# Performance work log

Hardware: AMD Instinct MI355X
Metric: run time of the kernel (lower is better)

The kernel has to match this reference:

```python
import jax, jax.numpy as jnp
import numpy as np

TAU = 10.0
EPS = 1e-6
TOP_K = 8


def setup_inputs() -> dict:
    key = jax.random.key(0)
    ks = jax.random.split(key, 5)
    D, NB, H = 1024, 512, 4096
    B, S = 4, 2048
    x = jax.random.normal(ks[0], (B, S, D), dtype=jnp.float32)
    W1 = jax.random.normal(ks[1], (H, D), dtype=jnp.float32) * (1.0 / np.sqrt(D))
    W2 = jax.random.normal(ks[2], (D, H), dtype=jnp.float32) * (1.0 / np.sqrt(H))
    ln_g = jnp.ones((D,), jnp.float32)
    ln_b = jnp.zeros((D,), jnp.float32)
    router_W = jax.random.normal(ks[3], (NB, D), dtype=jnp.float32) * 0.01
    router_b = jnp.zeros((NB,), jnp.float32)
    raw_U = jax.random.normal(ks[4], (NB, D), dtype=jnp.float32) * 0.02
    raw_V = jax.random.normal(jax.random.fold_in(key, 7), (NB, D), dtype=jnp.float32) * 0.02
    gamma = jnp.ones((1, 1, D), jnp.float32) * 0.1
    return {"x": x, "W1": W1, "W2": W2, "ln_g": ln_g, "ln_b": ln_b,
            "router_W": router_W, "router_b": router_b,
            "raw_U": raw_U, "raw_V": raw_V, "gamma": gamma}


def _layernorm(x, g, b):
    mu = jnp.mean(x, axis=-1, keepdims=True)
    var = jnp.var(x, axis=-1, keepdims=True)
    return (x - mu) * jax.lax.rsqrt(var + 1e-5) * g + b


def _unit_rows(W):
    n = jnp.linalg.norm(W, axis=1, keepdims=True)
    return W / jnp.maximum(n, EPS)


def reference(x, W1, W2, ln_g, ln_b, router_W, router_b, raw_U, raw_V, gamma):
    B, S, D = x.shape
    x_flat = x.reshape(-1, D)                      # [N, D]
    r_raw = _layernorm(x_flat, ln_g, ln_b) @ router_W.T + router_b  # [N, NB]
    r = jnp.clip(r_raw, -TAU, TAU)
    alpha = jax.nn.softplus(r)
    phi, idx = jax.lax.top_k(alpha, TOP_K)         # [N, K]
    S_sum = jnp.sum(phi, axis=-1, keepdims=True)
    Z = (phi / (S_sum + EPS)) * jnp.tanh(S_sum)    # [N, K]
    U_sel = _unit_rows(raw_U)[idx]                 # [N, K, D]
    V_sel = _unit_rows(raw_V)[idx]                 # [N, K, D]
    h_lat = jnp.einsum('nd,nkd->nk', x_flat, U_sel)
    dyn = jnp.einsum('nk,nkd->nd', h_lat * Z, V_sel).reshape(B, S, D) * gamma
    static = (jax.nn.gelu(x_flat @ W1.T, approximate=False) @ W2.T).reshape(B, S, D)
    return static + dyn
```

## Files before the change

### kernel.cpp

```cpp
#include <hip/hip_runtime.h>
#include <hip/hip_bf16.h>
#include <math.h>

#define N_TOK 8192
#define DDIM  1024
#define HDIM  4096
#define NBLK  512

typedef __bf16 bf16x8 __attribute__((ext_vector_type(8)));
typedef __bf16 bf16x4 __attribute__((ext_vector_type(4)));
typedef float  floatx4 __attribute__((ext_vector_type(4)));

__device__ __forceinline__ float wave_reduce_sum(float v) {
#pragma unroll
    for (int off = 32; off > 0; off >>= 1) v += __shfl_down(v, off, 64);
    return v;
}

__device__ __forceinline__ void gload_lds16(const void* g, void* l) {
    __builtin_amdgcn_global_load_lds((const __attribute__((address_space(1))) void*)g,
                                     (__attribute__((address_space(3))) void*)l,
                                     16, 0, 0);
}

__device__ __forceinline__ float fast_gelu(float x) {
    float ax = fabsf(x);
    float z  = ax * 0.70710678118654752f;
    float t  = __builtin_amdgcn_rcpf(fmaf(0.3275911f, z, 1.0f));
    float p  = fmaf(fmaf(fmaf(fmaf(1.061405429f, t, -1.453152027f),
                              t, 1.421413741f),
                         t, -0.284496736f),
                    t, 0.254829592f);
    p *= t;
    float e = __expf(-z * z);
    float E = fmaf(-p, e, 1.0f);
    return 0.5f * fmaf(ax, E, x);
}

__device__ __forceinline__ float fast_softplus(float r) {
    return __logf(fmaf(1.0f, __expf(r), 1.0f));
}

__device__ __forceinline__ void cast1024(const float* __restrict__ s,
                                         __bf16* __restrict__ d,
                                         size_t off, int t) {
    float4 v = ((const float4*)(s + off))[t];
    bf16x4 o;
    o.x = (__bf16)v.x; o.y = (__bf16)v.y;
    o.z = (__bf16)v.z; o.w = (__bf16)v.w;
    ((bf16x4*)(d + off))[t] = o;
}

__global__ __launch_bounds__(256) void prep_kernel(
        const float* __restrict__ x,
        const float* __restrict__ ln_g, const float* __restrict__ ln_b,
        const float* __restrict__ W1,   const float* __restrict__ W2,
        const float* __restrict__ router_W,
        const float* __restrict__ rawU, const float* __restrict__ rawV,
        __bf16* __restrict__ xb,  __bf16* __restrict__ lnb,
        __bf16* __restrict__ w1b, __bf16* __restrict__ w2b,
        __bf16* __restrict__ rwb,
        float* __restrict__ unitU, float* __restrict__ unitV) {
    int b = blockIdx.x;
    int t = threadIdx.x;

    if (b < 1024) {
        const float* src = (b < NBLK) ? rawU + (size_t)b * DDIM
                                      : rawV + (size_t)(b - NBLK) * DDIM;
        float* dst = (b < NBLK) ? unitU + (size_t)b * DDIM
                                : unitV + (size_t)(b - NBLK) * DDIM;
        float vals[4];
        float ss = 0.f;
#pragma unroll
        for (int i = 0; i < 4; i++) { vals[i] = src[t + i * 256]; ss += vals[i] * vals[i]; }
        __shared__ float red[4];
        ss = wave_reduce_sum(ss);
        if ((t & 63) == 0) red[t >> 6] = ss;
        __syncthreads();
        float tot = red[0] + red[1] + red[2] + red[3];
        float inv = 1.f / fmaxf(sqrtf(tot), 1e-6f);
#pragma unroll
        for (int i = 0; i < 4; i++) dst[t + i * 256] = vals[i] * inv;
    } else if (b < 9216) {
        int n = b - 1024;
        const float* row = x + (size_t)n * DDIM;
        float v[4];
        float s1 = 0.f, s2 = 0.f;
#pragma unroll
        for (int i = 0; i < 4; i++) {
            v[i] = row[t + i * 256];
            s1 += v[i];
            s2 += v[i] * v[i];
        }
        __shared__ float r1[4], r2[4];
        s1 = wave_reduce_sum(s1);
        s2 = wave_reduce_sum(s2);
        if ((t & 63) == 0) { r1[t >> 6] = s1; r2[t >> 6] = s2; }
        __syncthreads();
        float mu  = (r1[0] + r1[1] + r1[2] + r1[3]) * (1.f / DDIM);
        float var = (r2[0] + r2[1] + r2[2] + r2[3]) * (1.f / DDIM) - mu * mu;
        float rstd = rsqrtf(var + 1e-5f);
        __bf16* orow = lnb + (size_t)n * DDIM;
        __bf16* xrow = xb  + (size_t)n * DDIM;
#pragma unroll
        for (int i = 0; i < 4; i++) {
            int d = t + i * 256;
            orow[d] = (__bf16)((v[i] - mu) * rstd * ln_g[d] + ln_b[d]);
            xrow[d] = (__bf16)v[i];
        }
    } else if (b < 13312) {
        cast1024(W1, w1b, (size_t)(b - 9216) * 1024, t);
    } else if (b < 17408) {
        cast1024(W2, w2b, (size_t)(b - 13312) * 1024, t);
    } else {
        cast1024(router_W, rwb, (size_t)(b - 17408) * 1024, t);
    }
}

template <int MODE, int BN>
__global__ __launch_bounds__(256) void mfma_gemm(const __bf16* __restrict__ A,
                                                 const __bf16* __restrict__ B,
                                                 const float* __restrict__ bias,
                                                 void* __restrict__ Cv,
                                                 int M, int Nn, int Kk) {
    constexpr int NJ  = BN / 32;
    constexpr int NQB = BN / 64;
    __shared__ __align__(16) __bf16 As[2][128 * 32];
    __shared__ __align__(16) __bf16 Bs[2][BN * 32];

    const int t    = threadIdx.x;
    const int lane = t & 63;
    const int wave = t >> 6;
    const int wm   = wave >> 1, wn = wave & 1;
    const int lr   = lane & 15, quad = lane >> 4;
    const int m0   = blockIdx.x * 128;
    const int n0   = blockIdx.y * BN;

    const int ca0 = t & 3;
    const __bf16* Ag[2];
    const __bf16* Bg[NQB];
    int ldsOffA[2], ldsOffB[NQB];
#pragma unroll
    for (int q = 0; q < 2; q++) {
        int idx = q * 256 + t;
        Ag[q]      = A + (size_t)(m0 + (idx >> 2)) * Kk + ca0 * 8;
        ldsOffA[q] = idx * 8;
    }
#pragma unroll
    for (int q = 0; q < NQB; q++) {
        int idx = q * 256 + t;
        Bg[q]      = B + (size_t)(n0 + (idx >> 2)) * Kk + ca0 * 8;
        ldsOffB[q] = idx * 8;
    }

    int raOff[4], rbOff[NJ];
#pragma unroll
    for (int i = 0; i < 4; i++)
        raOff[i] = (wm * 64 + i * 16 + lr) * 32 + quad * 8;
#pragma unroll
    for (int j = 0; j < NJ; j++)
        rbOff[j] = (wn * (BN / 2) + j * 16 + lr) * 32 + quad * 8;

    floatx4 acc[4][NJ];
#pragma unroll
    for (int i = 0; i < 4; i++)
#pragma unroll
        for (int j = 0; j < NJ; j++) acc[i][j] = (floatx4)0.f;

#pragma unroll
    for (int q = 0; q < 2; q++)   gload_lds16(Ag[q], &As[0][ldsOffA[q]]);
#pragma unroll
    for (int q = 0; q < NQB; q++) gload_lds16(Bg[q], &Bs[0][ldsOffB[q]]);

    const int niter = Kk >> 5;
    for (int it = 0; it < niter; ++it) {
        const int cur = it & 1;
        __syncthreads();
        if (it + 1 < niter) {
            const int nk = (it + 1) << 5;
            const int nb = cur ^ 1;
#pragma unroll
            for (int q = 0; q < 2; q++)   gload_lds16(Ag[q] + nk, &As[nb][ldsOffA[q]]);
#pragma unroll
            for (int q = 0; q < NQB; q++) gload_lds16(Bg[q] + nk, &Bs[nb][ldsOffB[q]]);
        }
        bf16x8 af[4], bfr[NJ];
#pragma unroll
        for (int i = 0; i < 4; i++)  af[i]  = *(const bf16x8*)&As[cur][raOff[i]];
#pragma unroll
        for (int j = 0; j < NJ; j++) bfr[j] = *(const bf16x8*)&Bs[cur][rbOff[j]];
#pragma unroll
        for (int i = 0; i < 4; i++)
#pragma unroll
            for (int j = 0; j < NJ; j++)
                acc[i][j] = __builtin_amdgcn_mfma_f32_16x16x32_bf16(af[i], bfr[j],
                                                                    acc[i][j], 0, 0, 0);
    }

    const int mBase = m0 + wm * 64 + quad * 4;
    const int nBase = n0 + wn * (BN / 2) + lr;
#pragma unroll
    for (int i = 0; i < 4; i++) {
#pragma unroll
        for (int j = 0; j < NJ; j++) {
            int n = nBase + j * 16;
#pragma unroll
            for (int r = 0; r < 4; r++) {
                int m = mBase + i * 16 + r;
                float v = acc[i][j][r];
                if (MODE == 0) {
                    float rr = v + bias[n];
                    rr = fminf(fmaxf(rr, -10.f), 10.f);
                    ((float*)Cv)[(size_t)m * Nn + n] = fast_softplus(rr);
                } else if (MODE == 1) {
                    ((__bf16*)Cv)[(size_t)m * Nn + n] = (__bf16)fast_gelu(v);
                } else {
                    ((float*)Cv)[(size_t)m * Nn + n] += v;
                }
            }
        }
    }
}

__global__ __launch_bounds__(256) void topk_dyn_kernel(
        const float* __restrict__ alpha,
        const float* __restrict__ x,
        const float* __restrict__ unitU,
        const float* __restrict__ unitV,
        const float* __restrict__ gamma,
        float* __restrict__ out) {
    int n = blockIdx.x;
    int t = threadIdx.x;
    int lane = t & 63, wid = t >> 6;

    __shared__ int   sidx[8];
    __shared__ float shz[8];
    __shared__ float red[8][4];
    __shared__ float hz[8];

    if (wid == 0) {
        const float* row = alpha + (size_t)n * NBLK;
        float v[8];
#pragma unroll
        for (int i = 0; i < 8; i++) v[i] = row[lane + i * 64];
        float topv[8];
        int   topi[8];
        for (int s = 0; s < 8; s++) {
            float bv = v[0]; int bi = 0;
#pragma unroll
            for (int i = 1; i < 8; i++)
                if (v[i] > bv) { bv = v[i]; bi = i; }
            int gidx = lane + bi * 64;
#pragma unroll
            for (int off = 1; off < 64; off <<= 1) {
                float ov = __shfl_xor(bv, off, 64);
                int   oi = __shfl_xor(gidx, off, 64);
                if (ov > bv || (ov == bv && oi < gidx)) { bv = ov; gidx = oi; }
            }
            topv[s] = bv; topi[s] = gidx;
            if ((gidx & 63) == lane) v[gidx >> 6] = -1e30f;
        }
        float S = 0.f;
#pragma unroll
        for (int s = 0; s < 8; s++) S += topv[s];
        float zscale = tanhf(S) / (S + 1e-6f);
        if (lane < 8) {
            sidx[lane] = topi[lane];
            shz[lane]  = topv[lane] * zscale;
        }
    }
    __syncthreads();

    const float* xr = x + (size_t)n * DDIM;
    float xv[4];
#pragma unroll
    for (int i = 0; i < 4; i++) xv[i] = xr[t + i * 256];

    float acc[8];
#pragma unroll
    for (int k = 0; k < 8; k++) {
        const float* ur = unitU + (size_t)sidx[k] * DDIM;
        float a = 0.f;
#pragma unroll
        for (int i = 0; i < 4; i++) a = fmaf(xv[i], ur[t + i * 256], a);
        acc[k] = a;
    }
#pragma unroll
    for (int k = 0; k < 8; k++) {
        float a = wave_reduce_sum(acc[k]);
        if (lane == 0) red[k][wid] = a;
    }
    __syncthreads();
    if (t < 8) {
        float h = red[t][0] + red[t][1] + red[t][2] + red[t][3];
        hz[t] = h * shz[t];
    }
    __syncthreads();

    float* orow = out + (size_t)n * DDIM;
#pragma unroll
    for (int i = 0; i < 4; i++) {
        int d = t + i * 256;
        float s = 0.f;
#pragma unroll
        for (int k = 0; k < 8; k++)
            s = fmaf(hz[k], unitV[(size_t)sidx[k] * DDIM + d], s);
        orow[d] = s * gamma[d];
    }
}

extern "C" void kernel_launch(void* const* d_in, const int* in_sizes, int n_in,
                              void* d_out, int out_size, void* d_ws, size_t ws_size,
                              hipStream_t stream) {
    const float* x        = (const float*)d_in[0];
    const float* W1       = (const float*)d_in[1];
    const float* W2       = (const float*)d_in[2];
    const float* ln_g     = (const float*)d_in[3];
    const float* ln_b     = (const float*)d_in[4];
    const float* router_W = (const float*)d_in[5];
    const float* router_b = (const float*)d_in[6];
    const float* raw_U    = (const float*)d_in[7];
    const float* raw_V    = (const float*)d_in[8];
    const float* gamma    = (const float*)d_in[9];
    float* out = (float*)d_out;

    char* ws = (char*)d_ws;
    __bf16* lnb   = (__bf16*)(ws);
    float*  alpha = (float*)(ws + 16777216u);
    __bf16* g1    = (__bf16*)(ws);
    __bf16* xb    = (__bf16*)(ws + 67108864u);
    __bf16* w1b   = (__bf16*)(ws + 83886080u);
    __bf16* w2b   = (__bf16*)(ws + 92274688u);
    __bf16* rwb   = (__bf16*)(ws + 100663296u);
    float*  unitU = (float*)(ws + 101711872u);
    float*  unitV = (float*)(ws + 103809024u);

    prep_kernel<<<17920, 256, 0, stream>>>(x, ln_g, ln_b, W1, W2, router_W,
                                           raw_U, raw_V, xb, lnb, w1b, w2b, rwb,
                                           unitU, unitV);

    dim3 gR(N_TOK / 128, NBLK / 64);
    mfma_gemm<0, 64><<<gR, 256, 0, stream>>>(lnb, rwb, router_b, (void*)alpha,
                                             N_TOK, NBLK, DDIM);

    topk_dyn_kernel<<<N_TOK, 256, 0, stream>>>(alpha, x, unitU, unitV, gamma, out);

    dim3 g1d(N_TOK / 128, HDIM / 128);
    mfma_gemm<1, 128><<<g1d, 256, 0, stream>>>(xb, w1b, nullptr, (void*)g1,
                                               N_TOK, HDIM, DDIM);

    dim3 g2d(N_TOK / 128, DDIM / 64);
    mfma_gemm<2, 64><<<g2d, 256, 0, stream>>>(g1, w2b, nullptr, (void*)out,
                                              N_TOK, DDIM, HDIM);
}
```

Measured before the change: 378.2 us.

## Add 8-wave 256-row MFMA GEMM with quadrant pipelining for FFN matmuls

Adds a new 512-thread GEMM kernel that computes 256xBN output tiles, stages A and B halves into double-buffered LDS in four sub-steps interleaved with MFMA quadrants, and raises wave priority around the compute. It also remaps block IDs across 8 XCD chunks to improve L2 locality. Both FFN matmuls (W1 with GELU, W2 accumulate) switch to it, aiming for more reuse per loaded tile and overlap of global loads with compute. The larger tiles raise register and LDS pressure (up to 128 KB of LDS per block) and leave fewer blocks in the grid.

```diff
diff --git a/kernel.cpp b/kernel.cpp
--- a/kernel.cpp
+++ b/kernel.cpp
@@ -213,6 +213,171 @@
                     rr = fminf(fmaxf(rr, -10.f), 10.f);
                     ((float*)Cv)[(size_t)m * Nn + n] = fast_softplus(rr);
                 } else if (MODE == 1) {
+                    ((__bf16*)Cv)[(size_t)m * Nn + n] = (__bf16)fast_gelu(v);
+                } else {
+                    ((float*)Cv)[(size_t)m * Nn + n] += v;
+                }
+            }
+        }
+    }
+}
+
+template <int MODE, int BN>
+__global__ __launch_bounds__(512, 2) void mfma_gemm8(const __bf16* __restrict__ A,
+                                                     const __bf16* __restrict__ B,
+                                                     void* __restrict__ Cv,
+                                                     int M, int Nn, int Kk) {
+    constexpr int NJH    = BN / 128;
+    constexpr int NJ     = 2 * NJH;
+    constexpr int BCALLS = BN / 128;
+
+    __shared__ __align__(16) __bf16 As[2][256 * 64];
+    __shared__ __align__(16) __bf16 Bs[2][BN * 64];
+
+    const int t    = threadIdx.x;
+    const int lane = t & 63;
+    const int wave = t >> 6;
+    const int wm   = wave >> 2;
+    const int wn   = wave & 3;
+    const int lr   = lane & 15, quad = lane >> 4;
+
+    const int nbn   = Nn / BN;
+    const int chunk = gridDim.x >> 3;
+    const int bid   = blockIdx.x;
+    const int wg    = (bid & 7) * chunk + (bid >> 3);
+    const int m0    = (wg / nbn) * 256;
+    const int n0    = (wg % nbn) * BN;
+
+    const __bf16* aSrc[2][2]; int aDst[2][2];
+#pragma unroll
+    for (int q = 0; q < 2; q++) {
+        int idx = q * 512 + t;
+        int row = idx >> 3;
+        int cb  = ((idx & 7) << 4) ^ ((row & 7) << 4);
+#pragma unroll
+        for (int mh = 0; mh < 2; mh++) {
+            aSrc[q][mh] = A + (size_t)(m0 + mh * 128 + row) * Kk + (cb >> 1);
+            aDst[q][mh] = (mh * 128 + row) * 64 + (idx & 7) * 8;
+        }
+    }
+    const __bf16* bSrc[BCALLS][2]; int bDst[BCALLS][2];
+#pragma unroll
+    for (int q = 0; q < BCALLS; q++) {
+        int idx = q * 512 + t;
+        int row = idx >> 3;
+        int cb  = ((idx & 7) << 4) ^ ((row & 7) << 4);
+#pragma unroll
+        for (int nh = 0; nh < 2; nh++) {
+            bSrc[q][nh] = B + (size_t)(n0 + nh * (BN / 2) + row) * Kk + (cb >> 1);
+            bDst[q][nh] = (nh * (BN / 2) + row) * 64 + (idx & 7) * 8;
+        }
+    }
+
+    int aRd[2], bRd[2];
+#pragma unroll
+    for (int ks = 0; ks < 2; ks++) {
+        int sw = ((ks * 64 + quad * 16) ^ ((lr & 7) << 4)) >> 1;
+        aRd[ks] = (wm * 64 + lr) * 64 + sw;
+        bRd[ks] = (wn * (BN / 8) + lr) * 64 + sw;
+    }
+
+    floatx4 acc[8][NJ];
+#pragma unroll
+    for (int i = 0; i < 8; i++)
+#pragma unroll
+        for (int j = 0; j < NJ; j++) acc[i][j] = (floatx4)0.f;
+
+    bf16x8 af[4][2];
+    bf16x8 bfr[NJH][2];
+
+#define STAGE_A(KT, MH, BUF)                                                     \
+    _Pragma("unroll") for (int q = 0; q < 2; q++)                                \
+        gload_lds16(aSrc[q][MH] + (size_t)(KT) * 64, &As[BUF][aDst[q][MH]])
+#define STAGE_B(KT, NH, BUF)                                                     \
+    _Pragma("unroll") for (int q = 0; q < BCALLS; q++)                           \
+        gload_lds16(bSrc[q][NH] + (size_t)(KT) * 64, &Bs[BUF][bDst[q][NH]])
+#define LDA(MH)                                                                  \
+    _Pragma("unroll") for (int ii = 0; ii < 4; ii++)                             \
+    _Pragma("unroll") for (int ks = 0; ks < 2; ks++)                             \
+        af[ii][ks] = *(const bf16x8*)&As[cur][aRd[ks] + (MH) * 8192 + ii * 1024]
+#define LDB(NH)                                                                  \
+    _Pragma("unroll") for (int jj = 0; jj < NJH; jj++)                           \
+    _Pragma("unroll") for (int ks = 0; ks < 2; ks++)                             \
+        bfr[jj][ks] = *(const bf16x8*)&Bs[cur][bRd[ks] + ((NH) * (BN / 2) + jj * 16) * 64]
+#define MM(MH, NH)                                                               \
+    _Pragma("unroll") for (int ii = 0; ii < 4; ii++)                             \
+    _Pragma("unroll") for (int jj = 0; jj < NJH; jj++)                           \
+    _Pragma("unroll") for (int ks = 0; ks < 2; ks++)                             \
+        acc[(MH) * 4 + ii][(NH) * NJH + jj] =                                    \
+            __builtin_amdgcn_mfma_f32_16x16x32_bf16(                             \
+                af[ii][ks], bfr[jj][ks], acc[(MH) * 4 + ii][(NH) * NJH + jj],    \
+                0, 0, 0)
+#define WAITV()                                                                  \
+    do { if constexpr (BCALLS == 2) asm volatile("s_waitcnt vmcnt(4)" ::: "memory"); \
+         else                       asm volatile("s_waitcnt vmcnt(3)" ::: "memory"); } while (0)
+#define WAITL() asm volatile("s_waitcnt lgkmcnt(0)" ::: "memory")
+#define BARR()  __builtin_amdgcn_s_barrier()
+#define PRIO1() __builtin_amdgcn_s_setprio(1)
+#define PRIO0() __builtin_amdgcn_s_setprio(0)
+
+    const int NT = Kk >> 6;
+
+    STAGE_A(0, 0, 0);
+    STAGE_B(0, 0, 0);
+    STAGE_A(0, 1, 0);
+    STAGE_B(0, 1, 0);
+    WAITV();
+    BARR();
+
+    for (int kt = 0; kt < NT; ++kt) {
+        const int cur = kt & 1;
+        const int nxt = cur ^ 1;
+        const bool st = (kt + 1 < NT);
+        LDA(0); LDB(0);
+        if (st) STAGE_A(kt + 1, 0, nxt);
+        WAITV(); BARR(); WAITL();
+        PRIO1(); MM(0, 0); PRIO0();
+        BARR();
+        LDA(1);
+        if (st) STAGE_B(kt + 1, 0, nxt);
+        WAITV(); BARR(); WAITL();
+        PRIO1(); MM(1, 0); PRIO0();
+        BARR();
+        LDB(1);
+        if (st) STAGE_A(kt + 1, 1, nxt);
+        WAITV(); BARR(); WAITL();
+        PRIO1(); MM(1, 1); PRIO0();
+        BARR();
+        LDA(0);
+        if (st) STAGE_B(kt + 1, 1, nxt);
+        WAITV(); BARR(); WAITL();
+        PRIO1(); MM(0, 1); PRIO0();
+        BARR();
+    }
+
+#undef STAGE_A
+#undef STAGE_B
+#undef LDA
+#undef LDB
+#undef MM
+#undef WAITV
+#undef WAITL
+#undef BARR
+#undef PRIO1
+#undef PRIO0
+
+#pragma unroll
+    for (int i = 0; i < 8; i++) {
+        const int mh = i >> 2, ii = i & 3;
+#pragma unroll
+        for (int j = 0; j < NJ; j++) {
+            const int nh = j / NJH, jj = j % NJH;
+            const int n = n0 + nh * (BN / 2) + wn * (BN / 8) + jj * 16 + lr;
+#pragma unroll
+            for (int r = 0; r < 4; r++) {
+                const int m = m0 + mh * 128 + wm * 64 + ii * 16 + quad * 4 + r;
+                const float v = acc[i][j][r];
+                if (MODE == 1) {
                     ((__bf16*)Cv)[(size_t)m * Nn + n] = (__bf16)fast_gelu(v);
                 } else {
                     ((float*)Cv)[(size_t)m * Nn + n] += v;
@@ -345,11 +510,9 @@
 
     topk_dyn_kernel<<<N_TOK, 256, 0, stream>>>(alpha, x, unitU, unitV, gamma, out);
 
-    dim3 g1d(N_TOK / 128, HDIM / 128);
-    mfma_gemm<1, 128><<<g1d, 256, 0, stream>>>(xb, w1b, nullptr, (void*)g1,
-                                               N_TOK, HDIM, DDIM);
-
-    dim3 g2d(N_TOK / 128, DDIM / 64);
-    mfma_gemm<2, 64><<<g2d, 256, 0, stream>>>(g1, w2b, nullptr, (void*)out,
-                                              N_TOK, DDIM, HDIM);
-}
+    mfma_gemm8<1, 256><<<dim3(512), dim3(512), 0, stream>>>(xb, w1b, (void*)g1,
+                                                            N_TOK, HDIM, DDIM);
+
+    mfma_gemm8<2, 128><<<dim3(256), dim3(512), 0, stream>>>(g1, w2b, (void*)out,
+                                                            N_TOK, DDIM, HDIM);
+}
```

New measurement: 376.3 us. About the same (-0.5%).

## Replace FFN GEMMs with 256x256 8-wave pipelined MFMA kernel and split-K

Applied to the files above, without the earlier changes.

Adds a new 512-thread GEMM kernel with 256x256 tiles, double-buffered LDS via direct global-to-LDS loads, interleaved quarter-tile MFMA phases with wave priority hints, and XCD-aware block remapping. The W1 GEMM uses it directly with GELU, and the W2 GEMM uses split-K=2 with atomic adds into the output. The aim is more data reuse per tile and better overlap of loads with MFMA, which should raise matrix-core utilisation for the two big FFN GEMMs. The cost is large register and LDS use per block, and fp32 atomics that make the summation order nondeterministic.

```diff
diff --git a/kernel.cpp b/kernel.cpp
--- a/kernel.cpp
+++ b/kernel.cpp
@@ -216,6 +216,148 @@
                     ((__bf16*)Cv)[(size_t)m * Nn + n] = (__bf16)fast_gelu(v);
                 } else {
                     ((float*)Cv)[(size_t)m * Nn + n] += v;
+                }
+            }
+        }
+    }
+}
+
+template <int MODE, int SPLITK>
+__global__ __launch_bounds__(512, 2) void mfma_gemm8v2(const __bf16* __restrict__ A,
+                                                       const __bf16* __restrict__ B,
+                                                       void* __restrict__ Cv,
+                                                       int M, int Nn, int Kk) {
+    __shared__ __align__(16) __bf16 As[2][256 * 64];
+    __shared__ __align__(16) __bf16 Bs[2][256 * 64];
+
+    const int t    = threadIdx.x;
+    const int lane = t & 63;
+    const int wave = t >> 6;
+    const int wm   = wave >> 2;
+    const int wn   = wave & 3;
+    const int lr   = lane & 15, quad = lane >> 4;
+
+    const int nbn   = Nn >> 8;
+    const int nmb   = M >> 8;
+    const int chunk = gridDim.x >> 3;
+    const int bid   = blockIdx.x;
+    const int wg    = (bid & 7) * chunk + (bid >> 3);
+    const int kslc  = wg / (nmb * nbn);
+    const int rem   = wg % (nmb * nbn);
+    const int m0    = (rem / nbn) * 256;
+    const int n0    = (rem % nbn) * 256;
+    const int kseg  = Kk / SPLITK;
+    const int NT    = kseg >> 6;
+
+    const int srow = t >> 3;
+    const int scb  = ((t & 7) << 4) ^ ((srow & 7) << 4);
+    const __bf16* aP = A + (size_t)(m0 + srow) * Kk + (size_t)kslc * kseg + (scb >> 1);
+    const __bf16* bP = B + (size_t)(n0 + srow) * Kk + (size_t)kslc * kseg + (scb >> 1);
+    const int dP = srow * 64 + (t & 7) * 8;
+
+    int aRd[2], bRd[2];
+#pragma unroll
+    for (int ks = 0; ks < 2; ks++) {
+        int sw = ((ks * 64 + quad * 16) ^ ((lr & 7) << 4)) >> 1;
+        aRd[ks] = (wm * 64 + lr) * 64 + sw;
+        bRd[ks] = (wn * 32 + lr) * 64 + sw;
+    }
+
+    floatx4 acc[8][4];
+#pragma unroll
+    for (int i = 0; i < 8; i++)
+#pragma unroll
+        for (int j = 0; j < 4; j++) acc[i][j] = (floatx4)0.f;
+
+    bf16x8 af[4][2];
+    bf16x8 bfr0[2][2];
+    bf16x8 bfr1[2][2];
+
+#define STAGE_A(KT, MH, BUF)                                                        \
+    _Pragma("unroll") for (int q = 0; q < 2; q++)                                   \
+        gload_lds16(aP + (size_t)(KT) * 64 + (size_t)(q * 64 + (MH) * 128) * Kk,    \
+                    &As[BUF][dP + (q * 64 + (MH) * 128) * 64])
+#define STAGE_B(KT, NH, BUF)                                                        \
+    _Pragma("unroll") for (int q = 0; q < 2; q++)                                   \
+        gload_lds16(bP + (size_t)(KT) * 64 + (size_t)(q * 64 + (NH) * 128) * Kk,    \
+                    &Bs[BUF][dP + (q * 64 + (NH) * 128) * 64])
+#define LDA(CUR, MH)                                                                \
+    _Pragma("unroll") for (int ii = 0; ii < 4; ii++)                                \
+    _Pragma("unroll") for (int ks = 0; ks < 2; ks++)                                \
+        af[ii][ks] = *(const bf16x8*)&As[CUR][aRd[ks] + (MH) * 8192 + ii * 1024]
+#define LDB(CUR, NH, DST)                                                           \
+    _Pragma("unroll") for (int jj = 0; jj < 2; jj++)                                \
+    _Pragma("unroll") for (int ks = 0; ks < 2; ks++)                                \
+        DST[jj][ks] = *(const bf16x8*)&Bs[CUR][bRd[ks] + ((NH) * 128 + jj * 16) * 64]
+#define MM(MH, NH, BFR)                                                             \
+    _Pragma("unroll") for (int ii = 0; ii < 4; ii++)                                \
+    _Pragma("unroll") for (int jj = 0; jj < 2; jj++)                                \
+    _Pragma("unroll") for (int ks = 0; ks < 2; ks++)                                \
+        acc[(MH) * 4 + ii][(NH) * 2 + jj] =                                         \
+            __builtin_amdgcn_mfma_f32_16x16x32_bf16(                                \
+                af[ii][ks], BFR[jj][ks], acc[(MH) * 4 + ii][(NH) * 2 + jj], 0, 0, 0)
+#define VWAIT(NSTR) asm volatile("s_waitcnt vmcnt(" NSTR ")" ::: "memory")
+#define WAITL()     asm volatile("s_waitcnt lgkmcnt(0)" ::: "memory")
+#define BARR()      __builtin_amdgcn_s_barrier()
+#define PRIO1()     __builtin_amdgcn_s_setprio(1)
+#define PRIO0()     __builtin_amdgcn_s_setprio(0)
+
+#define TILE(KT, CUR, ST1, ST2, VM0, VM1, VM3)                                      \
+    do {                                                                            \
+        LDA(CUR, 0); LDB(CUR, 0, bfr0);                                             \
+        if (ST1) { STAGE_A((KT) + 1, 1, ((KT) + 1) & 1); }                          \
+        VWAIT(VM0); BARR(); WAITL();                                                \
+        PRIO1(); MM(0, 0, bfr0); PRIO0(); BARR();                                   \
+        LDB(CUR, 1, bfr1);                                                          \
+        if (ST2) { STAGE_A((KT) + 2, 0, (KT) & 1); }                                \
+        VWAIT(VM1); BARR(); WAITL();                                                \
+        PRIO1(); MM(0, 1, bfr1); PRIO0(); BARR();                                   \
+        LDA(CUR, 1);                                                                \
+        if (ST2) { STAGE_B((KT) + 2, 0, (KT) & 1); }                                \
+        BARR(); WAITL();                                                            \
+        PRIO1(); MM(1, 1, bfr1); PRIO0(); BARR();                                   \
+        if (ST2) { STAGE_B((KT) + 2, 1, (KT) & 1); }                                \
+        VWAIT(VM3); BARR();                                                         \
+        PRIO1(); MM(1, 0, bfr0); PRIO0(); BARR();                                   \
+    } while (0)
+
+    STAGE_A(0, 0, 0); STAGE_B(0, 0, 0); STAGE_B(0, 1, 0); STAGE_A(0, 1, 0);
+    STAGE_A(1, 0, 1); STAGE_B(1, 0, 1); STAGE_B(1, 1, 1);
+    VWAIT("10");
+    BARR();
+
+    for (int kt = 0; kt < NT - 2; ++kt)
+        TILE(kt, kt & 1, true, true, "10", "10", "10");
+    TILE(NT - 2, (NT - 2) & 1, true, false, "10", "8", "4");
+    TILE(NT - 1, (NT - 1) & 1, false, false, "2", "0", "0");
+
+#undef STAGE_A
+#undef STAGE_B
+#undef LDA
+#undef LDB
+#undef MM
+#undef VWAIT
+#undef WAITL
+#undef BARR
+#undef PRIO1
+#undef PRIO0
+#undef TILE
+
+#pragma unroll
+    for (int i = 0; i < 8; i++) {
+        const int mh = i >> 2, ii = i & 3;
+#pragma unroll
+        for (int j = 0; j < 4; j++) {
+            const int nh = j >> 1, jj = j & 1;
+            const int n = n0 + nh * 128 + wn * 32 + jj * 16 + lr;
+#pragma unroll
+            for (int r = 0; r < 4; r++) {
+                const int m = m0 + mh * 128 + wm * 64 + ii * 16 + quad * 4 + r;
+                const float v = acc[i][j][r];
+                if (MODE == 1) {
+                    ((__bf16*)Cv)[(size_t)m * Nn + n] = (__bf16)fast_gelu(v);
+                } else {
+                    atomicAdd(&((float*)Cv)[(size_t)m * Nn + n], v);
                 }
             }
         }
@@ -345,11 +487,9 @@
 
     topk_dyn_kernel<<<N_TOK, 256, 0, stream>>>(alpha, x, unitU, unitV, gamma, out);
 
-    dim3 g1d(N_TOK / 128, HDIM / 128);
-    mfma_gemm<1, 128><<<g1d, 256, 0, stream>>>(xb, w1b, nullptr, (void*)g1,
-                                               N_TOK, HDIM, DDIM);
-
-    dim3 g2d(N_TOK / 128, DDIM / 64);
-    mfma_gemm<2, 64><<<g2d, 256, 0, stream>>>(g1, w2b, nullptr, (void*)out,
-                                              N_TOK, DDIM, HDIM);
-}
+    mfma_gemm8v2<1, 1><<<dim3(512), dim3(512), 0, stream>>>(xb, w1b, (void*)g1,
+                                                            N_TOK, HDIM, DDIM);
+
+    mfma_gemm8v2<2, 2><<<dim3(256), dim3(512), 0, stream>>>(g1, w2b, (void*)out,
+                                                            N_TOK, DDIM, HDIM);
+}
```

New measurement: 364.0 us. 3.8% less time.

## Split-K the down-projection GEMM with atomics and vectorize elementwise kernels

Applied to the files above, without the earlier changes.

The second FFN GEMM now uses 128-wide N tiles with a 2-way split-K over the hidden dimension. The partial sums are accumulated into the output with atomicAdd, which keeps the block count the same while raising the work per block and reusing the A tile more. Separately, the prep, layernorm and top-k/dyn kernels switch to float4 and bf16x4 vector loads and stores. The atomics add contention and make the summation order nondeterministic.

```diff
diff --git a/kernel.cpp b/kernel.cpp
--- a/kernel.cpp
+++ b/kernel.cpp
@@ -69,29 +69,22 @@
                                       : rawV + (size_t)(b - NBLK) * DDIM;
         float* dst = (b < NBLK) ? unitU + (size_t)b * DDIM
                                 : unitV + (size_t)(b - NBLK) * DDIM;
-        float vals[4];
-        float ss = 0.f;
-#pragma unroll
-        for (int i = 0; i < 4; i++) { vals[i] = src[t + i * 256]; ss += vals[i] * vals[i]; }
+        float4 v = ((const float4*)src)[t];
+        float ss = v.x * v.x + v.y * v.y + v.z * v.z + v.w * v.w;
         __shared__ float red[4];
         ss = wave_reduce_sum(ss);
         if ((t & 63) == 0) red[t >> 6] = ss;
         __syncthreads();
         float tot = red[0] + red[1] + red[2] + red[3];
         float inv = 1.f / fmaxf(sqrtf(tot), 1e-6f);
-#pragma unroll
-        for (int i = 0; i < 4; i++) dst[t + i * 256] = vals[i] * inv;
+        float4 o;
+        o.x = v.x * inv; o.y = v.y * inv; o.z = v.z * inv; o.w = v.w * inv;
+        ((float4*)dst)[t] = o;
     } else if (b < 9216) {
         int n = b - 1024;
-        const float* row = x + (size_t)n * DDIM;
-        float v[4];
-        float s1 = 0.f, s2 = 0.f;
-#pragma unroll
-        for (int i = 0; i < 4; i++) {
-            v[i] = row[t + i * 256];
-            s1 += v[i];
-            s2 += v[i] * v[i];
-        }
+        float4 v = ((const float4*)(x + (size_t)n * DDIM))[t];
+        float s1 = v.x + v.y + v.z + v.w;
+        float s2 = v.x * v.x + v.y * v.y + v.z * v.z + v.w * v.w;
         __shared__ float r1[4], r2[4];
         s1 = wave_reduce_sum(s1);
         s2 = wave_reduce_sum(s2);
@@ -100,14 +93,17 @@
         float mu  = (r1[0] + r1[1] + r1[2] + r1[3]) * (1.f / DDIM);
         float var = (r2[0] + r2[1] + r2[2] + r2[3]) * (1.f / DDIM) - mu * mu;
         float rstd = rsqrtf(var + 1e-5f);
-        __bf16* orow = lnb + (size_t)n * DDIM;
-        __bf16* xrow = xb  + (size_t)n * DDIM;
-#pragma unroll
-        for (int i = 0; i < 4; i++) {
-            int d = t + i * 256;
-            orow[d] = (__bf16)((v[i] - mu) * rstd * ln_g[d] + ln_b[d]);
-            xrow[d] = (__bf16)v[i];
-        }
+        float4 g  = ((const float4*)ln_g)[t];
+        float4 bb = ((const float4*)ln_b)[t];
+        bf16x4 o, xo;
+        o.x = (__bf16)((v.x - mu) * rstd * g.x + bb.x);
+        o.y = (__bf16)((v.y - mu) * rstd * g.y + bb.y);
+        o.z = (__bf16)((v.z - mu) * rstd * g.z + bb.z);
+        o.w = (__bf16)((v.w - mu) * rstd * g.w + bb.w);
+        xo.x = (__bf16)v.x; xo.y = (__bf16)v.y;
+        xo.z = (__bf16)v.z; xo.w = (__bf16)v.w;
+        ((bf16x4*)(lnb + (size_t)n * DDIM))[t] = o;
+        ((bf16x4*)(xb  + (size_t)n * DDIM))[t] = xo;
     } else if (b < 13312) {
         cast1024(W1, w1b, (size_t)(b - 9216) * 1024, t);
     } else if (b < 17408) {
@@ -117,7 +113,7 @@
     }
 }
 
-template <int MODE, int BN>
+template <int MODE, int BN, int SPLITK>
 __global__ __launch_bounds__(256) void mfma_gemm(const __bf16* __restrict__ A,
                                                  const __bf16* __restrict__ B,
                                                  const float* __restrict__ bias,
@@ -135,6 +131,8 @@
     const int lr   = lane & 15, quad = lane >> 4;
     const int m0   = blockIdx.x * 128;
     const int n0   = blockIdx.y * BN;
+    const int kseg = Kk / SPLITK;
+    const int k0   = (SPLITK > 1) ? blockIdx.z * kseg : 0;
 
     const int ca0 = t & 3;
     const __bf16* Ag[2];
@@ -143,13 +141,13 @@
 #pragma unroll
     for (int q = 0; q < 2; q++) {
         int idx = q * 256 + t;
-        Ag[q]      = A + (size_t)(m0 + (idx >> 2)) * Kk + ca0 * 8;
+        Ag[q]      = A + (size_t)(m0 + (idx >> 2)) * Kk + k0 + ca0 * 8;
         ldsOffA[q] = idx * 8;
     }
 #pragma unroll
     for (int q = 0; q < NQB; q++) {
         int idx = q * 256 + t;
-        Bg[q]      = B + (size_t)(n0 + (idx >> 2)) * Kk + ca0 * 8;
+        Bg[q]      = B + (size_t)(n0 + (idx >> 2)) * Kk + k0 + ca0 * 8;
         ldsOffB[q] = idx * 8;
     }
 
@@ -172,7 +170,7 @@
 #pragma unroll
     for (int q = 0; q < NQB; q++) gload_lds16(Bg[q], &Bs[0][ldsOffB[q]]);
 
-    const int niter = Kk >> 5;
+    const int niter = kseg >> 5;
     for (int it = 0; it < niter; ++it) {
         const int cur = it & 1;
         __syncthreads();
@@ -215,7 +213,7 @@
                 } else if (MODE == 1) {
                     ((__bf16*)Cv)[(size_t)m * Nn + n] = (__bf16)fast_gelu(v);
                 } else {
-                    ((float*)Cv)[(size_t)m * Nn + n] += v;
+                    atomicAdd(&((float*)Cv)[(size_t)m * Nn + n], v);
                 }
             }
         }
@@ -271,19 +269,13 @@
     }
     __syncthreads();
 
-    const float* xr = x + (size_t)n * DDIM;
-    float xv[4];
-#pragma unroll
-    for (int i = 0; i < 4; i++) xv[i] = xr[t + i * 256];
+    float4 xv = ((const float4*)(x + (size_t)n * DDIM))[t];
 
     float acc[8];
 #pragma unroll
     for (int k = 0; k < 8; k++) {
-        const float* ur = unitU + (size_t)sidx[k] * DDIM;
-        float a = 0.f;
-#pragma unroll
-        for (int i = 0; i < 4; i++) a = fmaf(xv[i], ur[t + i * 256], a);
-        acc[k] = a;
+        float4 u = ((const float4*)(unitU + (size_t)sidx[k] * DDIM))[t];
+        acc[k] = xv.x * u.x + xv.y * u.y + xv.z * u.z + xv.w * u.w;
     }
 #pragma unroll
     for (int k = 0; k < 8; k++) {
@@ -297,16 +289,20 @@
     }
     __syncthreads();
 
-    float* orow = out + (size_t)n * DDIM;
-#pragma unroll
-    for (int i = 0; i < 4; i++) {
-        int d = t + i * 256;
-        float s = 0.f;
-#pragma unroll
-        for (int k = 0; k < 8; k++)
-            s = fmaf(hz[k], unitV[(size_t)sidx[k] * DDIM + d], s);
-        orow[d] = s * gamma[d];
-    }
+    float4 s = {0.f, 0.f, 0.f, 0.f};
+#pragma unroll
+    for (int k = 0; k < 8; k++) {
+        float4 v = ((const float4*)(unitV + (size_t)sidx[k] * DDIM))[t];
+        float h = hz[k];
+        s.x = fmaf(h, v.x, s.x);
+        s.y = fmaf(h, v.y, s.y);
+        s.z = fmaf(h, v.z, s.z);
+        s.w = fmaf(h, v.w, s.w);
+    }
+    float4 g = ((const float4*)gamma)[t];
+    float4 o;
+    o.x = s.x * g.x; o.y = s.y * g.y; o.z = s.z * g.z; o.w = s.w * g.w;
+    ((float4*)(out + (size_t)n * DDIM))[t] = o;
 }
 
 extern "C" void kernel_launch(void* const* d_in, const int* in_sizes, int n_in,
@@ -340,16 +336,16 @@
                                            unitU, unitV);
 
     dim3 gR(N_TOK / 128, NBLK / 64);
-    mfma_gemm<0, 64><<<gR, 256, 0, stream>>>(lnb, rwb, router_b, (void*)alpha,
-                                             N_TOK, NBLK, DDIM);
+    mfma_gemm<0, 64, 1><<<gR, 256, 0, stream>>>(lnb, rwb, router_b, (void*)alpha,
+                                                N_TOK, NBLK, DDIM);
 
     topk_dyn_kernel<<<N_TOK, 256, 0, stream>>>(alpha, x, unitU, unitV, gamma, out);
 
     dim3 g1d(N_TOK / 128, HDIM / 128);
-    mfma_gemm<1, 128><<<g1d, 256, 0, stream>>>(xb, w1b, nullptr, (void*)g1,
-                                               N_TOK, HDIM, DDIM);
-
-    dim3 g2d(N_TOK / 128, DDIM / 64);
-    mfma_gemm<2, 64><<<g2d, 256, 0, stream>>>(g1, w2b, nullptr, (void*)out,
-                                              N_TOK, DDIM, HDIM);
-}
+    mfma_gemm<1, 128, 1><<<g1d, 256, 0, stream>>>(xb, w1b, nullptr, (void*)g1,
+                                                  N_TOK, HDIM, DDIM);
+
+    dim3 g2d(N_TOK / 128, DDIM / 128, 2);
+    mfma_gemm<2, 128, 2><<<g2d, 256, 0, stream>>>(g1, w2b, nullptr, (void*)out,
+                                                  N_TOK, DDIM, HDIM);
+}
```

New measurement: 395.7 us. +4.6%, slower.
